# Performance work log

Measured on AMD Instinct MI355X. Metric: run time of the kernel, lower is better.

Reference implementation:

```python
import jax, jax.numpy as jnp
import numpy as np


def _l2norm(v, eps=1e-12):
    # torch F.normalize: v / max(||v||, eps)
    n = jnp.sqrt(jnp.sum(v * v, axis=-1, keepdims=True))
    return v / jnp.maximum(n, eps)


def setup_inputs() -> dict:
    key = jax.random.key(0)
    ks = jax.random.split(key, 5)
    B, D_in, D_out, N = 8192, 1024, 768, 16384
    x = jax.random.normal(ks[0], (B, D_in), dtype=jnp.float32)
    # Linear init ~ U(-1/sqrt(in), 1/sqrt(in)) in torch; scaled randn is fine for a numeric baseline
    W = jax.random.normal(ks[1], (D_out, D_in), dtype=jnp.float32) * (1.0 / np.sqrt(D_in))
    b = jax.random.normal(ks[2], (D_out,), dtype=jnp.float32) * 0.01
    # set_cache() stores L2-normalized keys/values
    cache_keys = _l2norm(jax.random.normal(ks[3], (N, D_out), dtype=jnp.float32))
    cache_values = _l2norm(jax.random.normal(ks[4], (N, D_out), dtype=jnp.float32))
    beta = jnp.asarray(5.0, dtype=jnp.float32)
    alpha = jnp.asarray(1.0, dtype=jnp.float32)
    return {"x": x, "W": W, "b": b, "cache_keys": cache_keys,
            "cache_values": cache_values, "beta": beta, "alpha": alpha}


def reference(x, W, b, cache_keys, cache_values, beta, alpha):
    # Linear projection: [B, D_in] @ [D_in, D_out] + b -> [B, D_out]
    projected = jnp.einsum("bi,oi->bo", x, W) + b
    # L2 normalize queries
    pn = _l2norm(projected)
    # Cosine similarity against cache keys: [B, N]
    similarity = jnp.einsum("bo,no->bn", pn, cache_keys)
    weights = jax.nn.softmax(beta * similarity, axis=-1)
    # Weighted cache read: [B, N] @ [N, D_out] -> [B, D_out]
    retrieved = jnp.einsum("bn,no->bo", weights, cache_values)
    return projected + alpha * retrieved
```

## Files before the change

kernel.cpp:

```cpp
#include <hip/hip_runtime.h>
#include <hip/hip_bf16.h>

typedef unsigned char  u8;
typedef unsigned short u16;
typedef unsigned int   u32;
typedef __attribute__((ext_vector_type(8)))  short bf16x8;
typedef __attribute__((ext_vector_type(4)))  float f32x4;
typedef __attribute__((ext_vector_type(4)))  int   i32x4;
typedef __attribute__((ext_vector_type(16))) int   i32x16;
typedef __attribute__((ext_vector_type(4)))  u16   u16x4;

__device__ __forceinline__ u16 f2bf(float f) {
  union { float f; u32 u; } v; v.f = f;
  u32 r = v.u + 0x7FFFu + ((v.u >> 16) & 1u);
  return (u16)(r >> 16);
}
__device__ __forceinline__ int q127(float x) { return (int)rintf(x * 127.0f); }

#define GLL16(gptr, lptr)                                                            \
  __builtin_amdgcn_global_load_lds((const __attribute__((address_space(1))) u32*)(gptr), \
                                   (__attribute__((address_space(3))) u32*)(lptr), 16, 0, 0)

#define BARRIER_LGKM() do { asm volatile("s_waitcnt lgkmcnt(0)" ::: "memory"); \
                            __builtin_amdgcn_s_barrier(); } while (0)

__global__ __launch_bounds__(256) void cvt_bf16(const float* __restrict__ in,
                                                u16* __restrict__ out, int n4) {
  int i = blockIdx.x * blockDim.x + threadIdx.x;
  int stride = gridDim.x * blockDim.x;
  for (; i < n4; i += stride) {
    float4 v = ((const float4*)in)[i];
    u16x4 o = { f2bf(v.x), f2bf(v.y), f2bf(v.z), f2bf(v.w) };
    ((u16x4*)out)[i] = o;
  }
}

__global__ __launch_bounds__(256) void buildK(const float* __restrict__ in,
                                              u8* __restrict__ out) {
  __shared__ float tile[64][65];
  int kt = blockIdx.x;
  int t = threadIdx.x;
  int r0 = t >> 6, c = t & 63;
  for (int dc = 0; dc < 12; ++dc) {
    if (dc) __syncthreads();
#pragma unroll
    for (int i = 0; i < 16; ++i) {
      int r = i * 4 + r0;
      tile[r][c] = in[(size_t)(kt * 64 + r) * 768 + dc * 64 + c];
    }
    __syncthreads();
    int d16l = t >> 6, key = t & 63;
    u32 wd[4];
#pragma unroll
    for (int g = 0; g < 4; ++g) {
      u32 v = 0;
#pragma unroll
      for (int j = 0; j < 4; ++j)
        v |= (u32)(q127(tile[key][d16l * 16 + g * 4 + j]) & 255) << (8 * j);
      wd[g] = v;
    }
    uint4 val = { wd[0], wd[1], wd[2], wd[3] };
    *(uint4*)(out + ((size_t)(dc * 4 + d16l) * 16384 + (size_t)(kt * 64 + key)) * 16) = val;
  }
}

__global__ __launch_bounds__(256) void buildV(const float* __restrict__ in,
                                              u8* __restrict__ out) {
  __shared__ float tile[64][65];
  int kt = blockIdx.x;
  int t = threadIdx.x;
  int r0 = t >> 6, c = t & 63;
  for (int dc = 0; dc < 12; ++dc) {
    if (dc) __syncthreads();
#pragma unroll
    for (int i = 0; i < 16; ++i) {
      int r = i * 4 + r0;
      tile[r][c] = in[(size_t)(kt * 64 + r) * 768 + dc * 64 + c];
    }
    __syncthreads();
    int k16l = t >> 6, dl = t & 63;
    u32 wd[4];
#pragma unroll
    for (int g = 0; g < 4; ++g) {
      u32 v = 0;
#pragma unroll
      for (int j = 0; j < 4; ++j)
        v |= (u32)(q127(tile[k16l * 16 + g * 4 + j][dl]) & 255) << (8 * j);
      wd[g] = v;
    }
    uint4 val = { wd[0], wd[1], wd[2], wd[3] };
    *(uint4*)(out + ((size_t)(kt * 4 + k16l) * 768 + (size_t)(dc * 64 + dl)) * 16) = val;
  }
}

__global__ __launch_bounds__(256) void gemm1(const u16* __restrict__ A,
                                             const u16* __restrict__ B,
                                             const float* __restrict__ bias,
                                             float* __restrict__ C) {
  __shared__ u16 As[2][128 * 32];
  __shared__ u16 Bs[2][128 * 32];
  int t = threadIdx.x;
  int brow = blockIdx.x * 128, bcol = blockIdx.y * 128;
  int w = t >> 6, l = t & 63;
  int l15 = l & 15, l4 = l >> 4;
  int wr = (w >> 1) * 64, wc = (w & 1) * 64;
  f32x4 acc[4][4];
#pragma unroll
  for (int i = 0; i < 4; ++i)
#pragma unroll
    for (int j = 0; j < 4; ++j) acc[i][j] = f32x4{0.f, 0.f, 0.f, 0.f};

  auto stage = [&](int buf, int kt) {
#pragma unroll
    for (int i = 0; i < 2; ++i) {
      int id = t + i * 256;
      int row = id >> 2, c = id & 3;
      int cs = (c ^ (row & 3)) * 8;
      GLL16(A + (size_t)(brow + row) * 1024 + kt * 32 + cs, &As[buf][id * 8]);
      GLL16(B + (size_t)(bcol + row) * 1024 + kt * 32 + cs, &Bs[buf][id * 8]);
    }
  };
  stage(0, 0);
  for (int kt = 0; kt < 32; ++kt) {
    int buf = kt & 1;
    __syncthreads();
    if (kt < 31) stage(buf ^ 1, kt + 1);
    bf16x8 a[4], b[4];
#pragma unroll
    for (int mf = 0; mf < 4; ++mf) {
      int row = wr + mf * 16 + l15;
      a[mf] = *(const bf16x8*)&As[buf][row * 32 + ((l4 ^ (row & 3)) * 8)];
    }
#pragma unroll
    for (int nf = 0; nf < 4; ++nf) {
      int row = wc + nf * 16 + l15;
      b[nf] = *(const bf16x8*)&Bs[buf][row * 32 + ((l4 ^ (row & 3)) * 8)];
    }
#pragma unroll
    for (int mf = 0; mf < 4; ++mf)
#pragma unroll
      for (int nf = 0; nf < 4; ++nf)
        acc[mf][nf] = __builtin_amdgcn_mfma_f32_16x16x32_bf16(a[mf], b[nf], acc[mf][nf], 0, 0, 0);
  }
#pragma unroll
  for (int mf = 0; mf < 4; ++mf)
#pragma unroll
    for (int nf = 0; nf < 4; ++nf) {
      int col = bcol + wc + nf * 16 + l15;
      float bv = bias[col];
#pragma unroll
      for (int j = 0; j < 4; ++j) {
        int row = brow + wr + mf * 16 + l4 * 4 + j;
        C[(size_t)row * 768 + col] = acc[mf][nf][j] + bv;
      }
    }
}

__global__ __launch_bounds__(384) void rownorm8(const float* __restrict__ P,
                                                u8* __restrict__ q8) {
  int row = blockIdx.x, t = threadIdx.x;
  size_t base = (size_t)row * 768;
  float2 v = *(const float2*)&P[base + 2 * t];
  float ss = v.x * v.x + v.y * v.y;
#pragma unroll
  for (int o = 32; o; o >>= 1) ss += __shfl_xor(ss, o);
  __shared__ float wsum[6];
  if ((t & 63) == 0) wsum[t >> 6] = ss;
  __syncthreads();
  float tot = wsum[0] + wsum[1] + wsum[2] + wsum[3] + wsum[4] + wsum[5];
  float inv = 1.0f / fmaxf(sqrtf(tot), 1e-12f);
  int a = q127(v.x * inv), b = q127(v.y * inv);
  *(u16*)(q8 + base + 2 * t) = (u16)((a & 255) | ((b & 255) << 8));
}

__global__ __launch_bounds__(1024, 4) void attn(const u8* __restrict__ q8,
                                                const u8* __restrict__ Ki8,
                                                const u8* __restrict__ Vi8,
                                                const float* __restrict__ beta_p,
                                                u16* __restrict__ Opart,
                                                float* __restrict__ lpart) {
  __shared__ i32x4 Qlds[48 * 64];
  __shared__ i32x4 Ps[2][32 * 64];
  __shared__ float lred[16][64];
  int t = threadIdx.x;
  int w = t >> 6, l = t & 63;
  int ql = l & 31, hi = l >> 5;
  int l15 = l & 15, l4g = l >> 4;
  int split = blockIdx.x, qb = blockIdx.y;
  int qrow0 = qb * 64;
  float beta = beta_p[0];
  float c1 = beta * 1.44269504089f / 16129.0f;
  float lg2ps = 6.98868468677f - beta * 1.44269504089f;
  float invps = expf(beta) / 127.0f;
  float ovs = expf(beta) / 16129.0f;

#pragma unroll
  for (int i = 0; i < 3; ++i) {
    int id = i * 1024 + t;
    int c16 = id >> 6, q = id & 63;
    Qlds[id] = *(const i32x4*)(q8 + (size_t)(qrow0 + q) * 768 + (size_t)c16 * 16);
  }

  i32x4 oacc[4][3];
#pragma unroll
  for (int mq = 0; mq < 4; ++mq)
#pragma unroll
    for (int nd = 0; nd < 3; ++nd) oacc[mq][nd] = i32x4{0, 0, 0, 0};
  int lsum0 = 0, lsum1 = 0;

  int kbase = split * 8192;
  const i32x4* Kp = (const i32x4*)Ki8 + (size_t)hi * 16384 + (size_t)(kbase + w * 32 + ql);
  const i32x4* Vp = (const i32x4*)Vi8 + ((size_t)(kbase >> 4) + l4g) * 768 + (size_t)(w * 48 + l15);

  i32x4 kb[3];
#pragma unroll
  for (int s = 0; s < 3; ++s) kb[s] = Kp[(size_t)(2 * s) * 16384];

  __syncthreads();

  for (int it = 0; it < 16; ++it) {
    int n0 = it * 512;
    const i32x4* kp = Kp + n0;
    i32x4* psb = &Ps[it & 1][0];

    i32x16 sacc0 = (i32x16)0;
    i32x16 sacc1 = (i32x16)0;
    __builtin_amdgcn_s_setprio(1);
#pragma unroll
    for (int ks = 0; ks < 24; ++ks) {
      i32x4 av = kb[ks % 3];
      if (ks < 21) kb[ks % 3] = kp[(size_t)(2 * (ks + 3)) * 16384];
      i32x4 q0 = Qlds[(2 * ks + hi) * 64 + ql];
      i32x4 q1 = Qlds[(2 * ks + hi) * 64 + ql + 32];
      sacc0 = __builtin_amdgcn_mfma_i32_32x32x32_i8(av, q0, sacc0, 0, 0, 0);
      sacc1 = __builtin_amdgcn_mfma_i32_32x32x32_i8(av, q1, sacc1, 0, 0, 0);
    }
    __builtin_amdgcn_s_setprio(0);

#pragma unroll
    for (int qf = 0; qf < 2; ++qf) {
      int q = ql + qf * 32;
      int lacc = 0;
#pragma unroll
      for (int rg = 0; rg < 4; ++rg) {
        float p0, p1, p2, p3;
        if (qf == 0) {
          p0 = exp2f(fmaf(c1, (float)sacc0[rg * 4 + 0], lg2ps));
          p1 = exp2f(fmaf(c1, (float)sacc0[rg * 4 + 1], lg2ps));
          p2 = exp2f(fmaf(c1, (float)sacc0[rg * 4 + 2], lg2ps));
          p3 = exp2f(fmaf(c1, (float)sacc0[rg * 4 + 3], lg2ps));
        } else {
          p0 = exp2f(fmaf(c1, (float)sacc1[rg * 4 + 0], lg2ps));
          p1 = exp2f(fmaf(c1, (float)sacc1[rg * 4 + 1], lg2ps));
          p2 = exp2f(fmaf(c1, (float)sacc1[rg * 4 + 2], lg2ps));
          p3 = exp2f(fmaf(c1, (float)sacc1[rg * 4 + 3], lg2ps));
        }
        int i0 = (int)rintf(fminf(p0, 127.f));
        int i1 = (int)rintf(fminf(p1, 127.f));
        int i2 = (int)rintf(fminf(p2, 127.f));
        int i3 = (int)rintf(fminf(p3, 127.f));
        u32 pk = (u32)i0 | ((u32)i1 << 8) | ((u32)i2 << 16) | ((u32)i3 << 24);
#if __has_builtin(__builtin_amdgcn_sdot4)
        lacc = __builtin_amdgcn_sdot4((int)pk, 0x01010101, lacc, false);
#else
        lacc += i0 + i1 + i2 + i3;
#endif
        ((u32*)psb)[((2 * w + (rg >> 1)) * 64 + q) * 4 + 2 * (rg & 1) + hi] = pk;
      }
      if (qf == 0) lsum0 += lacc; else lsum1 += lacc;
    }

    if (it < 15) {
      const i32x4* kpn = Kp + (size_t)(it + 1) * 512;
#pragma unroll
      for (int s = 0; s < 3; ++s) kb[s] = kpn[(size_t)(2 * s) * 16384];
    }
    i32x4 vb[2][3];
#pragma unroll
    for (int nd = 0; nd < 3; ++nd)
      vb[0][nd] = Vp[(size_t)(n0 >> 4) * 768 + nd * 16];

    BARRIER_LGKM();

    __builtin_amdgcn_s_setprio(1);
#pragma unroll
    for (int ksv = 0; ksv < 8; ++ksv) {
      int cur = ksv & 1;
      if (ksv < 7) {
#pragma unroll
        for (int nd = 0; nd < 3; ++nd)
          vb[cur ^ 1][nd] = Vp[((size_t)(n0 >> 4) + (ksv + 1) * 4) * 768 + nd * 16];
      }
#pragma unroll
      for (int mq = 0; mq < 4; ++mq) {
        i32x4 pa = psb[(4 * ksv + l4g) * 64 + mq * 16 + l15];
        oacc[mq][0] = __builtin_amdgcn_mfma_i32_16x16x64_i8(pa, vb[cur][0], oacc[mq][0], 0, 0, 0);
        oacc[mq][1] = __builtin_amdgcn_mfma_i32_16x16x64_i8(pa, vb[cur][1], oacc[mq][1], 0, 0, 0);
        oacc[mq][2] = __builtin_amdgcn_mfma_i32_16x16x64_i8(pa, vb[cur][2], oacc[mq][2], 0, 0, 0);
      }
    }
    __builtin_amdgcn_s_setprio(0);
  }

  {
    float s0 = (float)(lsum0 + __shfl_xor(lsum0, 32)) * invps;
    float s1 = (float)(lsum1 + __shfl_xor(lsum1, 32)) * invps;
    if (hi == 0) { lred[w][ql] = s0; lred[w][ql + 32] = s1; }
  }
  __syncthreads();
  if (t < 64) {
    float s = 0.f;
#pragma unroll
    for (int ww = 0; ww < 16; ++ww) s += lred[ww][t];
    lpart[split * 8192 + qrow0 + t] = s;
  }

#pragma unroll
  for (int mq = 0; mq < 4; ++mq)
#pragma unroll
    for (int nd = 0; nd < 3; ++nd) {
      int col = w * 48 + nd * 16 + l15;
#pragma unroll
      for (int j = 0; j < 4; ++j) {
        int row = qrow0 + mq * 16 + l4g * 4 + j;
        Opart[((size_t)split * 8192 + row) * 768 + col] = f2bf((float)oacc[mq][nd][j] * ovs);
      }
    }
}

__global__ __launch_bounds__(192) void combine(float* __restrict__ out,
                                               const u16* __restrict__ Opart,
                                               const float* __restrict__ lpart,
                                               const float* __restrict__ alpha_p) {
  int row = blockIdx.x, t = threadIdx.x;
  float scale = alpha_p[0] / (lpart[row] + lpart[8192 + row]);
  size_t base = (size_t)row * 768 + t * 4;
  u16x4 o0 = *(const u16x4*)&Opart[base];
  u16x4 o1 = *(const u16x4*)&Opart[(size_t)6291456 + base];
  float4 cur = *(float4*)&out[base];
  union { u32 u; float f; } c0, c1, c2, c3, d0_, d1_, d2_, d3_;
  c0.u = (u32)o0[0] << 16; c1.u = (u32)o0[1] << 16; c2.u = (u32)o0[2] << 16; c3.u = (u32)o0[3] << 16;
  d0_.u = (u32)o1[0] << 16; d1_.u = (u32)o1[1] << 16; d2_.u = (u32)o1[2] << 16; d3_.u = (u32)o1[3] << 16;
  cur.x += (c0.f + d0_.f) * scale;
  cur.y += (c1.f + d1_.f) * scale;
  cur.z += (c2.f + d2_.f) * scale;
  cur.w += (c3.f + d3_.f) * scale;
  *(float4*)&out[base] = cur;
}

extern "C" void kernel_launch(void* const* d_in, const int* in_sizes, int n_in,
                              void* d_out, int out_size, void* d_ws, size_t ws_size,
                              hipStream_t stream) {
  const float* x      = (const float*)d_in[0];
  const float* W      = (const float*)d_in[1];
  const float* bias   = (const float*)d_in[2];
  const float* keys   = (const float*)d_in[3];
  const float* values = (const float*)d_in[4];
  const float* beta   = (const float*)d_in[5];
  const float* alpha  = (const float*)d_in[6];
  float* out = (float*)d_out;

  char* ws = (char*)d_ws;
  u16* xb    = (u16*)(ws + 0);
  u16* Wb    = (u16*)(ws + 16777216);
  u8*  Ki8   = (u8*) (ws + 18350080);
  u8*  Vi8   = (u8*) (ws + 30932992);
  u8*  q8    = (u8*) (ws + 43515904);
  u16* Opart = (u16*)(ws + 49807360);
  float* lp  = (float*)(ws + 74973184);

  cvt_bf16<<<2048, 256, 0, stream>>>(x, xb, 8192 * 1024 / 4);
  cvt_bf16<<<768, 256, 0, stream>>>(W, Wb, 768 * 1024 / 4);
  buildK<<<256, 256, 0, stream>>>(keys, Ki8);
  buildV<<<256, 256, 0, stream>>>(values, Vi8);
  gemm1<<<dim3(64, 6), 256, 0, stream>>>(xb, Wb, bias, out);
  rownorm8<<<8192, 384, 0, stream>>>(out, q8);
  attn<<<dim3(2, 128), 1024, 0, stream>>>(q8, Ki8, Vi8, beta, Opart, lp);
  combine<<<8192, 192, 0, stream>>>(out, Opart, lp, alpha);
}
```

Baseline: 282.0 us.

## Software-pipeline PV MFMA of previous tile behind current tile's exp/quantize

Restructures the main loop so the P·V matrix multiply for tile it-1 runs right after the QK MFMAs of tile it, before the exp/quantize softmax step. A final epilogue handles the last tile. The aim is to overlap transcendental/VALU softmax work with MFMA work and to hide the barrier latency, using the existing double-buffered Ps. The cost is more live registers (the vb buffers are hoisted) and a dependence on the double buffering being correct across the single barrier per iteration.

New measurement: 302.5 us. +7.3%, slower.

```diff
diff --git a/kernel.cpp b/kernel.cpp
--- a/kernel.cpp
+++ b/kernel.cpp
@@ -216,6 +216,8 @@
 #pragma unroll
   for (int s = 0; s < 3; ++s) kb[s] = Kp[(size_t)(2 * s) * 16384];
 
+  i32x4 vb[2][3];
+
   __syncthreads();
 
   for (int it = 0; it < 16; ++it) {
@@ -236,6 +238,35 @@
       sacc1 = __builtin_amdgcn_mfma_i32_32x32x32_i8(av, q1, sacc1, 0, 0, 0);
     }
     __builtin_amdgcn_s_setprio(0);
+
+    if (it < 15) {
+      const i32x4* kpn = Kp + (size_t)(it + 1) * 512;
+#pragma unroll
+      for (int s = 0; s < 3; ++s) kb[s] = kpn[(size_t)(2 * s) * 16384];
+    }
+
+    if (it > 0) {
+      int m0 = (it - 1) * 512;
+      i32x4* psp = &Ps[(it - 1) & 1][0];
+      __builtin_amdgcn_s_setprio(1);
+#pragma unroll
+      for (int ksv = 0; ksv < 8; ++ksv) {
+        int cur = ksv & 1;
+        if (ksv < 7) {
+#pragma unroll
+          for (int nd = 0; nd < 3; ++nd)
+            vb[cur ^ 1][nd] = Vp[((size_t)(m0 >> 4) + (ksv + 1) * 4) * 768 + nd * 16];
+        }
+#pragma unroll
+        for (int mq = 0; mq < 4; ++mq) {
+          i32x4 pa = psp[(4 * ksv + l4g) * 64 + mq * 16 + l15];
+          oacc[mq][0] = __builtin_amdgcn_mfma_i32_16x16x64_i8(pa, vb[cur][0], oacc[mq][0], 0, 0, 0);
+          oacc[mq][1] = __builtin_amdgcn_mfma_i32_16x16x64_i8(pa, vb[cur][1], oacc[mq][1], 0, 0, 0);
+          oacc[mq][2] = __builtin_amdgcn_mfma_i32_16x16x64_i8(pa, vb[cur][2], oacc[mq][2], 0, 0, 0);
+        }
+      }
+      __builtin_amdgcn_s_setprio(0);
+    }
 
 #pragma unroll
     for (int qf = 0; qf < 2; ++qf) {
@@ -270,18 +301,16 @@
       if (qf == 0) lsum0 += lacc; else lsum1 += lacc;
     }
 
-    if (it < 15) {
-      const i32x4* kpn = Kp + (size_t)(it + 1) * 512;
-#pragma unroll
-      for (int s = 0; s < 3; ++s) kb[s] = kpn[(size_t)(2 * s) * 16384];
-    }
-    i32x4 vb[2][3];
 #pragma unroll
     for (int nd = 0; nd < 3; ++nd)
       vb[0][nd] = Vp[(size_t)(n0 >> 4) * 768 + nd * 16];
 
     BARRIER_LGKM();
-
+  }
+
+  {
+    int m0 = 15 * 512;
+    i32x4* psp = &Ps[15 & 1][0];
     __builtin_amdgcn_s_setprio(1);
 #pragma unroll
     for (int ksv = 0; ksv < 8; ++ksv) {
@@ -289,11 +318,11 @@
       if (ksv < 7) {
 #pragma unroll
         for (int nd = 0; nd < 3; ++nd)
-          vb[cur ^ 1][nd] = Vp[((size_t)(n0 >> 4) + (ksv + 1) * 4) * 768 + nd * 16];
+          vb[cur ^ 1][nd] = Vp[((size_t)(m0 >> 4) + (ksv + 1) * 4) * 768 + nd * 16];
       }
 #pragma unroll
       for (int mq = 0; mq < 4; ++mq) {
-        i32x4 pa = psb[(4 * ksv + l4g) * 64 + mq * 16 + l15];
+        i32x4 pa = psp[(4 * ksv + l4g) * 64 + mq * 16 + l15];
         oacc[mq][0] = __builtin_amdgcn_mfma_i32_16x16x64_i8(pa, vb[cur][0], oacc[mq][0], 0, 0, 0);
         oacc[mq][1] = __builtin_amdgcn_mfma_i32_16x16x64_i8(pa, vb[cur][1], oacc[mq][1], 0, 0, 0);
         oacc[mq][2] = __builtin_amdgcn_mfma_i32_16x16x64_i8(pa, vb[cur][2], oacc[mq][2], 0, 0, 0);
```
